# Optimization experiments

Measured on AMD Instinct MI355X. Metric: run time of the kernel, lower is better.

Reference implementation:

```python
import jax, jax.numpy as jnp
import numpy as np

B, C, D = 4, 512, 1024
N = 8           # num_experts
DFF = 4096      # GEGLU inner dim; in-projection outputs 2*DFF


def setup_inputs() -> dict:
    key = jax.random.key(0)
    ks = jax.random.split(key, 7)
    hidden_states = jax.random.normal(ks[0], (B, C, D), dtype=jnp.float32)
    # Dispatch mask: one-hot expert assignment per token (top-1 routing).
    assign = jax.random.randint(ks[1], (B, C), 0, N)
    dispatch_mask = jax.nn.one_hot(assign, N, dtype=jnp.float32)        # [B,C,N]
    # Combine mask: same sparsity pattern, scaled by a router probability.
    probs = jax.random.uniform(ks[2], (B, C, 1), dtype=jnp.float32)
    combine_mask = dispatch_mask * probs                                 # [B,C,N]
    s_in = 1.0 / np.sqrt(D)
    s_out = 1.0 / np.sqrt(DFF)
    W_in = jax.random.normal(ks[3], (N, 2 * DFF, D), dtype=jnp.float32) * s_in
    b_in = jax.random.normal(ks[4], (N, 2 * DFF), dtype=jnp.float32) * 0.01
    W_out = jax.random.normal(ks[5], (N, D, DFF), dtype=jnp.float32) * s_out
    b_out = jax.random.normal(ks[6], (N, D), dtype=jnp.float32) * 0.01
    return {"hidden_states": hidden_states, "dispatch_mask": dispatch_mask,
            "combine_mask": combine_mask, "W_in": W_in, "b_in": b_in,
            "W_out": W_out, "b_out": b_out}


def reference(hidden_states, dispatch_mask, combine_mask, W_in, b_in, W_out, b_out):
    # Dispatch: [B,C,D] x [B,C,N] -> [N,B,C,D]
    h = jnp.einsum('bcd,bcn->nbcd', hidden_states, dispatch_mask)
    # Per-expert GEGLU FFN.
    h = jnp.einsum('nbcd,nfd->nbcf', h, W_in) + b_in[:, None, None, :]   # [N,B,C,2*DFF]
    x, gate = jnp.split(h, 2, axis=-1)
    h = x * jax.nn.gelu(gate, approximate=False)                          # torch F.gelu = exact erf
    h = jnp.einsum('nbcd,nfd->nbcf', h, W_out) + b_out[:, None, None, :]  # [N,B,C,D]
    # Combine: [N,B,C,D] x [B,C,N] -> [B,C,D]
    return jnp.einsum('nbcd,bcn->bcd', h, combine_mask)
```

## Files before the change

kernel.cpp:

```cpp
#include <hip/hip_runtime.h>
#include <math.h>

#define NTOK 2048
#define DDIM 1024
#define NEXP 8
#define DFF 4096
#define TWODFF 8192

typedef __attribute__((ext_vector_type(8))) short bf16x8;
typedef __attribute__((ext_vector_type(4))) short bf16x4;
typedef __attribute__((ext_vector_type(4))) float f32x4;

__device__ __forceinline__ short f2bf(float f) {
  unsigned u = __builtin_bit_cast(unsigned, f);
  u = (u + 0x7FFFu + ((u >> 16) & 1u)) >> 16;
  return (short)u;
}

__device__ __forceinline__ unsigned pk2(float a, float b) {
  unsigned r;
  asm("v_cvt_pk_bf16_f32 %0, %1, %2" : "=v"(r) : "v"(a), "v"(b));
  return r;
}

__global__ void route_k(const float* __restrict__ disp, const float* __restrict__ comb,
                        int* __restrict__ cnt, int* __restrict__ tokl,
                        float* __restrict__ scale) {
  __shared__ int lcnt[NEXP];
  const int tid = threadIdx.x;
  if (tid < NEXP) lcnt[tid] = 0;
  __syncthreads();
  for (int i = 0; i < 8; ++i) {
    const int t = i * 256 + tid;
    const float* row = disp + (size_t)t * NEXP;
    int e = 0;
#pragma unroll
    for (int n = 1; n < NEXP; ++n) e = (row[n] > row[e]) ? n : e;
    const float p = comb[(size_t)t * NEXP + e];
    const int slot = atomicAdd(&lcnt[e], 1);
    tokl[e * NTOK + slot] = t;
    scale[t] = p;
  }
  __syncthreads();
  if (tid < NEXP) cnt[tid] = lcnt[tid];
}

__global__ __launch_bounds__(256) void gemm1_k(
    const float* __restrict__ hid, const float* __restrict__ Win,
    const float* __restrict__ bin, const int* __restrict__ cnt,
    const int* __restrict__ tokl, short* __restrict__ act) {
  const int e = blockIdx.z;
  const int Me = cnt[e];
  const int m0 = blockIdx.y * 128;
  if (m0 >= Me) return;
  const int f0 = blockIdx.x * 64;

  __shared__ short Al[2][128 * 32];
  __shared__ short Bl[2][128 * 32];
  __shared__ int tokids[128];

  const int tid = threadIdx.x;
  if (tid < 128) {
    const int r = m0 + tid;
    tokids[tid] = (r < Me) ? tokl[e * NTOK + r] : -1;
  }
  __syncthreads();

  const int r0 = tid >> 3;
  const int c0 = (tid & 7) * 4;
  const float* aP[4];
  const float* bP[4];
#pragma unroll
  for (int i = 0; i < 4; ++i) {
    const int row = i * 32 + r0;
    const int tk = tokids[row];
    aP[i] = (tk >= 0) ? (hid + (size_t)tk * DDIM + c0) : nullptr;
    const int wr = (row < 64) ? (f0 + row) : (DFF + f0 + (row - 64));
    bP[i] = Win + (size_t)e * TWODFF * DDIM + (size_t)wr * DDIM + c0;
  }

  float4 aR[4], bR[4];
  auto load_t = [&](int k0) {
#pragma unroll
    for (int i = 0; i < 4; ++i) {
      bR[i] = *(const float4*)(bP[i] + k0);
      aR[i] = aP[i] ? *(const float4*)(aP[i] + k0) : make_float4(0.f, 0.f, 0.f, 0.f);
    }
  };
  auto store_t = [&](int buf) {
#pragma unroll
    for (int i = 0; i < 4; ++i) {
      const int row = i * 32 + r0;
      const int ba = (row * 64 + (tid & 7) * 8) ^ ((row & 7) << 4);
      uint2 va, vb;
      va.x = pk2(aR[i].x, aR[i].y); va.y = pk2(aR[i].z, aR[i].w);
      vb.x = pk2(bR[i].x, bR[i].y); vb.y = pk2(bR[i].z, bR[i].w);
      *(uint2*)((char*)Al[buf] + ba) = va;
      *(uint2*)((char*)Bl[buf] + ba) = vb;
    }
  };

  const int wid = tid >> 6, lane = tid & 63;
  const int wm = (wid >> 1) * 64;
  const int wf = (wid & 1) * 32;
  const int lr = lane & 15;
  const int kbyte = (lane >> 4) * 16;

  f32x4 accx[4][2], accg[4][2];
  const f32x4 zf = {0.f, 0.f, 0.f, 0.f};
#pragma unroll
  for (int a = 0; a < 4; ++a)
#pragma unroll
    for (int b = 0; b < 2; ++b) { accx[a][b] = zf; accg[a][b] = zf; }

  load_t(0);
  store_t(0);

  for (int kt = 0; kt < 32; ++kt) {
    if (kt < 31) load_t((kt + 1) * 32);
    __syncthreads();
    const char* Ab = (const char*)Al[kt & 1];
    const char* Bb = (const char*)Bl[kt & 1];
    bf16x8 a[4], bx[2], bg[2];
#pragma unroll
    for (int fm = 0; fm < 4; ++fm) {
      const int row = wm + fm * 16 + lr;
      a[fm] = *(const bf16x8*)(Ab + ((row * 64 + kbyte) ^ ((row & 7) << 4)));
    }
#pragma unroll
    for (int ff = 0; ff < 2; ++ff) {
      const int rx = wf + ff * 16 + lr;
      bx[ff] = *(const bf16x8*)(Bb + ((rx * 64 + kbyte) ^ ((rx & 7) << 4)));
      const int rg = rx + 64;
      bg[ff] = *(const bf16x8*)(Bb + ((rg * 64 + kbyte) ^ ((rg & 7) << 4)));
    }
#pragma unroll
    for (int fm = 0; fm < 4; ++fm)
#pragma unroll
      for (int ff = 0; ff < 2; ++ff) {
        accx[fm][ff] = __builtin_amdgcn_mfma_f32_16x16x32_bf16(a[fm], bx[ff], accx[fm][ff], 0, 0, 0);
        accg[fm][ff] = __builtin_amdgcn_mfma_f32_16x16x32_bf16(a[fm], bg[ff], accg[fm][ff], 0, 0, 0);
      }
    if (kt < 31) store_t((kt + 1) & 1);
  }

  const int orb = (lane >> 4) * 4;
#pragma unroll
  for (int ff = 0; ff < 2; ++ff) {
    const int fcol = f0 + wf + ff * 16 + lr;
    const float bx_ = bin[e * TWODFF + fcol];
    const float bg_ = bin[e * TWODFF + DFF + fcol];
#pragma unroll
    for (int fm = 0; fm < 4; ++fm)
#pragma unroll
      for (int j = 0; j < 4; ++j) {
        const int row = wm + fm * 16 + orb + j;
        if (m0 + row < Me) {
          const float x = accx[fm][ff][j] + bx_;
          const float g = accg[fm][ff][j] + bg_;
          const float gl = 0.5f * g * (1.f + erff(g * 0.70710678118654752f));
          act[(size_t)tokids[row] * DFF + fcol] = f2bf(x * gl);
        }
      }
  }
}

__global__ __launch_bounds__(256) void gemm2_k(
    const short* __restrict__ act, const float* __restrict__ Wout,
    const float* __restrict__ bout, const int* __restrict__ cnt,
    const int* __restrict__ tokl, const float* __restrict__ scale,
    float* __restrict__ out) {
  const int e = blockIdx.z;
  const int Me = cnt[e];
  const int m0 = blockIdx.y * 128;
  if (m0 >= Me) return;
  const int n0 = blockIdx.x * 64;

  __shared__ short Al[2][128 * 64];
  __shared__ short Bl[2][64 * 64];
  __shared__ int tokids[128];
  __shared__ float pv[128];

  const int tid = threadIdx.x;
  if (tid < 128) {
    const int r = m0 + tid;
    const int tk = (r < Me) ? tokl[e * NTOK + r] : -1;
    tokids[tid] = tk;
    pv[tid] = (tk >= 0) ? scale[tk] : 0.f;
  }
  __syncthreads();

  const int ar0 = tid >> 3;
  const int ac0 = (tid & 7) * 8;
  const short* aP[4];
#pragma unroll
  for (int i = 0; i < 4; ++i) {
    const int row = i * 32 + ar0;
    const int tk = tokids[row];
    aP[i] = (tk >= 0) ? (act + (size_t)tk * DFF + ac0) : nullptr;
  }
  const int br0 = tid >> 4;
  const int bc0 = (tid & 15) * 4;
  const float* bP[4];
#pragma unroll
  for (int i = 0; i < 4; ++i) {
    const int row = i * 16 + br0;
    bP[i] = Wout + (size_t)e * DDIM * DFF + (size_t)(n0 + row) * DFF + bc0;
  }

  bf16x8 aR[4];
  float4 bR[4];
  auto load_t = [&](int k0) {
#pragma unroll
    for (int i = 0; i < 4; ++i) bR[i] = *(const float4*)(bP[i] + k0);
    const bf16x8 z = {0, 0, 0, 0, 0, 0, 0, 0};
#pragma unroll
    for (int i = 0; i < 4; ++i) aR[i] = aP[i] ? *(const bf16x8*)(aP[i] + k0) : z;
  };
  auto store_t = [&](int buf) {
#pragma unroll
    for (int i = 0; i < 4; ++i) {
      const int row = i * 32 + ar0;
      const int ba = (row * 128 + (tid & 7) * 16) ^ ((row & 7) << 4);
      *(bf16x8*)((char*)Al[buf] + ba) = aR[i];
    }
#pragma unroll
    for (int i = 0; i < 4; ++i) {
      const int row = i * 16 + br0;
      const int bb = (row * 128 + (tid & 15) * 8) ^ ((row & 7) << 4);
      uint2 vb;
      vb.x = pk2(bR[i].x, bR[i].y); vb.y = pk2(bR[i].z, bR[i].w);
      *(uint2*)((char*)Bl[buf] + bb) = vb;
    }
  };

  const int wid = tid >> 6, lane = tid & 63;
  const int wm = (wid >> 1) * 64;
  const int wn = (wid & 1) * 32;
  const int lr = lane & 15;
  const int lkb = (lane >> 4) * 16;

  f32x4 acc[4][2];
  const f32x4 zf = {0.f, 0.f, 0.f, 0.f};
#pragma unroll
  for (int a = 0; a < 4; ++a) { acc[a][0] = zf; acc[a][1] = zf; }

  load_t(0);
  store_t(0);

  for (int kt = 0; kt < 64; ++kt) {
    if (kt < 63) load_t((kt + 1) * 64);
    __syncthreads();
    const char* Ab = (const char*)Al[kt & 1];
    const char* Bb = (const char*)Bl[kt & 1];
#pragma unroll
    for (int ks = 0; ks < 2; ++ks) {
      bf16x8 a[4], b[2];
      const int kb = ks * 64 + lkb;
#pragma unroll
      for (int fm = 0; fm < 4; ++fm) {
        const int row = wm + fm * 16 + lr;
        a[fm] = *(const bf16x8*)(Ab + ((row * 128 + kb) ^ ((row & 7) << 4)));
      }
#pragma unroll
      for (int ff = 0; ff < 2; ++ff) {
        const int rn = wn + ff * 16 + lr;
        b[ff] = *(const bf16x8*)(Bb + ((rn * 128 + kb) ^ ((rn & 7) << 4)));
      }
#pragma unroll
      for (int fm = 0; fm < 4; ++fm)
#pragma unroll
        for (int ff = 0; ff < 2; ++ff)
          acc[fm][ff] = __builtin_amdgcn_mfma_f32_16x16x32_bf16(a[fm], b[ff], acc[fm][ff], 0, 0, 0);
    }
    if (kt < 63) store_t((kt + 1) & 1);
  }

  const int orb = (lane >> 4) * 4;
#pragma unroll
  for (int ff = 0; ff < 2; ++ff) {
    const int ncol = n0 + wn + ff * 16 + lr;
    const float bo = bout[e * DDIM + ncol];
#pragma unroll
    for (int fm = 0; fm < 4; ++fm)
#pragma unroll
      for (int j = 0; j < 4; ++j) {
        const int row = wm + fm * 16 + orb + j;
        if (m0 + row < Me)
          out[(size_t)tokids[row] * DDIM + ncol] = pv[row] * (acc[fm][ff][j] + bo);
      }
  }
}

extern "C" void kernel_launch(void* const* d_in, const int* in_sizes, int n_in,
                              void* d_out, int out_size, void* d_ws, size_t ws_size,
                              hipStream_t stream) {
  const float* hid = (const float*)d_in[0];
  const float* disp = (const float*)d_in[1];
  const float* comb = (const float*)d_in[2];
  const float* Win = (const float*)d_in[3];
  const float* bin = (const float*)d_in[4];
  const float* Wout = (const float*)d_in[5];
  const float* bout = (const float*)d_in[6];
  float* out = (float*)d_out;

  char* ws = (char*)d_ws;
  int* cnt = (int*)(ws);
  int* tokl = (int*)(ws + 256);
  float* scale = (float*)(ws + 256 + NTOK * NEXP * 4);
  short* act = (short*)(ws + (1 << 17));

  route_k<<<1, 256, 0, stream>>>(disp, comb, cnt, tokl, scale);
  gemm1_k<<<dim3(DFF / 64, 4, NEXP), 256, 0, stream>>>(hid, Win, bin, cnt, tokl, act);
  gemm2_k<<<dim3(DDIM / 64, 4, NEXP), 256, 0, stream>>>(act, Wout, bout, cnt, tokl, scale, out);
}
```

Baseline: 203.8 us.

## Enlarge expert GEMM tiles to 256 rows with 512 threads and interleave experts

Both expert GEMMs now use 512-thread blocks covering 256 token rows: 256x128 x/gate columns in the first GEMM and 256x64 in the second. The block index is remapped so consecutive blocks cycle across experts. Since roughly 256 tokens land on each expert, each weight tile is streamed by fewer row-blocks, cutting redundant fp32 weight traffic. The cost is fewer, larger blocks and higher register pressure in the first GEMM; when an expert has slightly more than 256 tokens, a second block still reads full weight tiles for few rows.

```diff
diff --git a/kernel.cpp b/kernel.cpp
--- a/kernel.cpp
+++ b/kernel.cpp
@@ -8,7 +8,6 @@
 #define TWODFF 8192
 
 typedef __attribute__((ext_vector_type(8))) short bf16x8;
-typedef __attribute__((ext_vector_type(4))) short bf16x4;
 typedef __attribute__((ext_vector_type(4))) float f32x4;
 
 __device__ __forceinline__ short f2bf(float f) {
@@ -45,22 +44,24 @@
   if (tid < NEXP) cnt[tid] = lcnt[tid];
 }
 
-__global__ __launch_bounds__(256) void gemm1_k(
+__global__ __launch_bounds__(512) void gemm1_k(
     const float* __restrict__ hid, const float* __restrict__ Win,
     const float* __restrict__ bin, const int* __restrict__ cnt,
     const int* __restrict__ tokl, short* __restrict__ act) {
-  const int e = blockIdx.z;
+  const int bid = blockIdx.x + 32 * (blockIdx.y + 2 * blockIdx.z);
+  const int e = bid & 7;
+  const int rem = bid >> 3;
+  const int f0 = (rem & 31) * 128;
+  const int m0 = (rem >> 5) * 256;
   const int Me = cnt[e];
-  const int m0 = blockIdx.y * 128;
   if (m0 >= Me) return;
-  const int f0 = blockIdx.x * 64;
-
-  __shared__ short Al[2][128 * 32];
-  __shared__ short Bl[2][128 * 32];
-  __shared__ int tokids[128];
+
+  __shared__ short Al[2][256 * 32];
+  __shared__ short Bl[2][256 * 32];
+  __shared__ int tokids[256];
 
   const int tid = threadIdx.x;
-  if (tid < 128) {
+  if (tid < 256) {
     const int r = m0 + tid;
     tokids[tid] = (r < Me) ? tokl[e * NTOK + r] : -1;
   }
@@ -72,10 +73,10 @@
   const float* bP[4];
 #pragma unroll
   for (int i = 0; i < 4; ++i) {
-    const int row = i * 32 + r0;
+    const int row = i * 64 + r0;
     const int tk = tokids[row];
     aP[i] = (tk >= 0) ? (hid + (size_t)tk * DDIM + c0) : nullptr;
-    const int wr = (row < 64) ? (f0 + row) : (DFF + f0 + (row - 64));
+    const int wr = (row < 128) ? (f0 + row) : (DFF + f0 + (row - 128));
     bP[i] = Win + (size_t)e * TWODFF * DDIM + (size_t)wr * DDIM + c0;
   }
 
@@ -90,7 +91,7 @@
   auto store_t = [&](int buf) {
 #pragma unroll
     for (int i = 0; i < 4; ++i) {
-      const int row = i * 32 + r0;
+      const int row = i * 64 + r0;
       const int ba = (row * 64 + (tid & 7) * 8) ^ ((row & 7) << 4);
       uint2 va, vb;
       va.x = pk2(aR[i].x, aR[i].y); va.y = pk2(aR[i].z, aR[i].w);
@@ -101,15 +102,15 @@
   };
 
   const int wid = tid >> 6, lane = tid & 63;
-  const int wm = (wid >> 1) * 64;
-  const int wf = (wid & 1) * 32;
+  const int mi = wid >> 2;
+  const int fi = wid & 3;
   const int lr = lane & 15;
   const int kbyte = (lane >> 4) * 16;
 
-  f32x4 accx[4][2], accg[4][2];
+  f32x4 accx[8][2], accg[8][2];
   const f32x4 zf = {0.f, 0.f, 0.f, 0.f};
 #pragma unroll
-  for (int a = 0; a < 4; ++a)
+  for (int a = 0; a < 8; ++a)
 #pragma unroll
     for (int b = 0; b < 2; ++b) { accx[a][b] = zf; accg[a][b] = zf; }
 
@@ -121,21 +122,21 @@
     __syncthreads();
     const char* Ab = (const char*)Al[kt & 1];
     const char* Bb = (const char*)Bl[kt & 1];
-    bf16x8 a[4], bx[2], bg[2];
-#pragma unroll
-    for (int fm = 0; fm < 4; ++fm) {
-      const int row = wm + fm * 16 + lr;
+    bf16x8 a[8], bx[2], bg[2];
+#pragma unroll
+    for (int fm = 0; fm < 8; ++fm) {
+      const int row = mi * 128 + fm * 16 + lr;
       a[fm] = *(const bf16x8*)(Ab + ((row * 64 + kbyte) ^ ((row & 7) << 4)));
     }
 #pragma unroll
     for (int ff = 0; ff < 2; ++ff) {
-      const int rx = wf + ff * 16 + lr;
+      const int rx = fi * 32 + ff * 16 + lr;
       bx[ff] = *(const bf16x8*)(Bb + ((rx * 64 + kbyte) ^ ((rx & 7) << 4)));
-      const int rg = rx + 64;
+      const int rg = rx + 128;
       bg[ff] = *(const bf16x8*)(Bb + ((rg * 64 + kbyte) ^ ((rg & 7) << 4)));
     }
 #pragma unroll
-    for (int fm = 0; fm < 4; ++fm)
+    for (int fm = 0; fm < 8; ++fm)
 #pragma unroll
       for (int ff = 0; ff < 2; ++ff) {
         accx[fm][ff] = __builtin_amdgcn_mfma_f32_16x16x32_bf16(a[fm], bx[ff], accx[fm][ff], 0, 0, 0);
@@ -147,14 +148,14 @@
   const int orb = (lane >> 4) * 4;
 #pragma unroll
   for (int ff = 0; ff < 2; ++ff) {
-    const int fcol = f0 + wf + ff * 16 + lr;
+    const int fcol = f0 + fi * 32 + ff * 16 + lr;
     const float bx_ = bin[e * TWODFF + fcol];
     const float bg_ = bin[e * TWODFF + DFF + fcol];
 #pragma unroll
-    for (int fm = 0; fm < 4; ++fm)
+    for (int fm = 0; fm < 8; ++fm)
 #pragma unroll
       for (int j = 0; j < 4; ++j) {
-        const int row = wm + fm * 16 + orb + j;
+        const int row = mi * 128 + fm * 16 + orb + j;
         if (m0 + row < Me) {
           const float x = accx[fm][ff][j] + bx_;
           const float g = accg[fm][ff][j] + bg_;
@@ -165,24 +166,26 @@
   }
 }
 
-__global__ __launch_bounds__(256) void gemm2_k(
+__global__ __launch_bounds__(512) void gemm2_k(
     const short* __restrict__ act, const float* __restrict__ Wout,
     const float* __restrict__ bout, const int* __restrict__ cnt,
     const int* __restrict__ tokl, const float* __restrict__ scale,
     float* __restrict__ out) {
-  const int e = blockIdx.z;
+  const int bid = blockIdx.x + 16 * (blockIdx.y + 2 * blockIdx.z);
+  const int e = bid & 7;
+  const int rem = bid >> 3;
+  const int n0 = (rem & 15) * 64;
+  const int m0 = (rem >> 4) * 256;
   const int Me = cnt[e];
-  const int m0 = blockIdx.y * 128;
   if (m0 >= Me) return;
-  const int n0 = blockIdx.x * 64;
-
-  __shared__ short Al[2][128 * 64];
+
+  __shared__ short Al[2][256 * 64];
   __shared__ short Bl[2][64 * 64];
-  __shared__ int tokids[128];
-  __shared__ float pv[128];
+  __shared__ int tokids[256];
+  __shared__ float pv[256];
 
   const int tid = threadIdx.x;
-  if (tid < 128) {
+  if (tid < 256) {
     const int r = m0 + tid;
     const int tk = (r < Me) ? tokl[e * NTOK + r] : -1;
     tokids[tid] = tk;
@@ -191,28 +194,26 @@
   __syncthreads();
 
   const int ar0 = tid >> 3;
-  const int ac0 = (tid & 7) * 8;
   const short* aP[4];
 #pragma unroll
   for (int i = 0; i < 4; ++i) {
-    const int row = i * 32 + ar0;
+    const int row = i * 64 + ar0;
     const int tk = tokids[row];
-    aP[i] = (tk >= 0) ? (act + (size_t)tk * DFF + ac0) : nullptr;
+    aP[i] = (tk >= 0) ? (act + (size_t)tk * DFF + (tid & 7) * 8) : nullptr;
   }
   const int br0 = tid >> 4;
-  const int bc0 = (tid & 15) * 4;
-  const float* bP[4];
-#pragma unroll
-  for (int i = 0; i < 4; ++i) {
-    const int row = i * 16 + br0;
-    bP[i] = Wout + (size_t)e * DDIM * DFF + (size_t)(n0 + row) * DFF + bc0;
+  const float* bP[2];
+#pragma unroll
+  for (int i = 0; i < 2; ++i) {
+    const int row = i * 32 + br0;
+    bP[i] = Wout + (size_t)e * DDIM * DFF + (size_t)(n0 + row) * DFF + (tid & 15) * 4;
   }
 
   bf16x8 aR[4];
-  float4 bR[4];
+  float4 bR[2];
   auto load_t = [&](int k0) {
 #pragma unroll
-    for (int i = 0; i < 4; ++i) bR[i] = *(const float4*)(bP[i] + k0);
+    for (int i = 0; i < 2; ++i) bR[i] = *(const float4*)(bP[i] + k0);
     const bf16x8 z = {0, 0, 0, 0, 0, 0, 0, 0};
 #pragma unroll
     for (int i = 0; i < 4; ++i) aR[i] = aP[i] ? *(const bf16x8*)(aP[i] + k0) : z;
@@ -220,13 +221,13 @@
   auto store_t = [&](int buf) {
 #pragma unroll
     for (int i = 0; i < 4; ++i) {
-      const int row = i * 32 + ar0;
+      const int row = i * 64 + ar0;
       const int ba = (row * 128 + (tid & 7) * 16) ^ ((row & 7) << 4);
       *(bf16x8*)((char*)Al[buf] + ba) = aR[i];
     }
 #pragma unroll
-    for (int i = 0; i < 4; ++i) {
-      const int row = i * 16 + br0;
+    for (int i = 0; i < 2; ++i) {
+      const int row = i * 32 + br0;
       const int bb = (row * 128 + (tid & 15) * 8) ^ ((row & 7) << 4);
       uint2 vb;
       vb.x = pk2(bR[i].x, bR[i].y); vb.y = pk2(bR[i].z, bR[i].w);
@@ -235,8 +236,8 @@
   };
 
   const int wid = tid >> 6, lane = tid & 63;
-  const int wm = (wid >> 1) * 64;
-  const int wn = (wid & 1) * 32;
+  const int mi = wid >> 1;
+  const int di = wid & 1;
   const int lr = lane & 15;
   const int lkb = (lane >> 4) * 16;
 
@@ -259,12 +260,12 @@
       const int kb = ks * 64 + lkb;
 #pragma unroll
       for (int fm = 0; fm < 4; ++fm) {
-        const int row = wm + fm * 16 + lr;
+        const int row = mi * 64 + fm * 16 + lr;
         a[fm] = *(const bf16x8*)(Ab + ((row * 128 + kb) ^ ((row & 7) << 4)));
       }
 #pragma unroll
       for (int ff = 0; ff < 2; ++ff) {
-        const int rn = wn + ff * 16 + lr;
+        const int rn = di * 32 + ff * 16 + lr;
         b[ff] = *(const bf16x8*)(Bb + ((rn * 128 + kb) ^ ((rn & 7) << 4)));
       }
 #pragma unroll
@@ -279,13 +280,13 @@
   const int orb = (lane >> 4) * 4;
 #pragma unroll
   for (int ff = 0; ff < 2; ++ff) {
-    const int ncol = n0 + wn + ff * 16 + lr;
+    const int ncol = n0 + di * 32 + ff * 16 + lr;
     const float bo = bout[e * DDIM + ncol];
 #pragma unroll
     for (int fm = 0; fm < 4; ++fm)
 #pragma unroll
       for (int j = 0; j < 4; ++j) {
-        const int row = wm + fm * 16 + orb + j;
+        const int row = mi * 64 + fm * 16 + orb + j;
         if (m0 + row < Me)
           out[(size_t)tokids[row] * DDIM + ncol] = pv[row] * (acc[fm][ff][j] + bo);
       }
@@ -311,6 +312,6 @@
   short* act = (short*)(ws + (1 << 17));
 
   route_k<<<1, 256, 0, stream>>>(disp, comb, cnt, tokl, scale);
-  gemm1_k<<<dim3(DFF / 64, 4, NEXP), 256, 0, stream>>>(hid, Win, bin, cnt, tokl, act);
-  gemm2_k<<<dim3(DDIM / 64, 4, NEXP), 256, 0, stream>>>(act, Wout, bout, cnt, tokl, scale, out);
-}
+  gemm1_k<<<dim3(32, 2, NEXP), 512, 0, stream>>>(hid, Win, bin, cnt, tokl, act);
+  gemm2_k<<<dim3(16, 2, NEXP), 512, 0, stream>>>(act, Wout, bout, cnt, tokl, scale, out);
+}
```

After: 201.9 us. Within noise of the previous version (-0.9%).

## Deepen gemm1 prefetch to triple-buffered LDS with two register stages

Applied to the files above, without the earlier changes.

The gemm1 kernel moves from double-buffered LDS with a one-tile-ahead register prefetch to three LDS buffers and two alternating register sets, so global loads are issued two k-tiles ahead. The aim is to hide more global-memory latency behind the MFMA work. It also adds a launch-bounds minimum of 3 blocks per CU, which limits registers, and it increases LDS use and register pressure, with a risk of spills. The gemm2 change is a cosmetic inlining of an offset.

```diff
diff --git a/kernel.cpp b/kernel.cpp
--- a/kernel.cpp
+++ b/kernel.cpp
@@ -8,7 +8,6 @@
 #define TWODFF 8192
 
 typedef __attribute__((ext_vector_type(8))) short bf16x8;
-typedef __attribute__((ext_vector_type(4))) short bf16x4;
 typedef __attribute__((ext_vector_type(4))) float f32x4;
 
 __device__ __forceinline__ short f2bf(float f) {
@@ -45,7 +44,25 @@
   if (tid < NEXP) cnt[tid] = lcnt[tid];
 }
 
-__global__ __launch_bounds__(256) void gemm1_k(
+#define G1_LOAD(aR, bR, k0) do {                                              \
+  _Pragma("unroll") for (int i_ = 0; i_ < 4; ++i_) {                          \
+    bR[i_] = *(const float4*)(bP[i_] + (k0));                                 \
+    aR[i_] = aP[i_] ? *(const float4*)(aP[i_] + (k0))                         \
+                    : make_float4(0.f, 0.f, 0.f, 0.f);                        \
+  } } while (0)
+
+#define G1_STORE(aR, bR, buf) do {                                            \
+  _Pragma("unroll") for (int i_ = 0; i_ < 4; ++i_) {                          \
+    const int row_ = i_ * 32 + r0;                                            \
+    const int ba_ = (row_ * 64 + (tid & 7) * 8) ^ ((row_ & 7) << 4);          \
+    uint2 va_, vb_;                                                           \
+    va_.x = pk2(aR[i_].x, aR[i_].y); va_.y = pk2(aR[i_].z, aR[i_].w);         \
+    vb_.x = pk2(bR[i_].x, bR[i_].y); vb_.y = pk2(bR[i_].z, bR[i_].w);         \
+    *(uint2*)((char*)Al[buf] + ba_) = va_;                                    \
+    *(uint2*)((char*)Bl[buf] + ba_) = vb_;                                    \
+  } } while (0)
+
+__global__ __launch_bounds__(256, 3) void gemm1_k(
     const float* __restrict__ hid, const float* __restrict__ Win,
     const float* __restrict__ bin, const int* __restrict__ cnt,
     const int* __restrict__ tokl, short* __restrict__ act) {
@@ -55,8 +72,8 @@
   if (m0 >= Me) return;
   const int f0 = blockIdx.x * 64;
 
-  __shared__ short Al[2][128 * 32];
-  __shared__ short Bl[2][128 * 32];
+  __shared__ short Al[3][128 * 32];
+  __shared__ short Bl[3][128 * 32];
   __shared__ int tokids[128];
 
   const int tid = threadIdx.x;
@@ -79,27 +96,6 @@
     bP[i] = Win + (size_t)e * TWODFF * DDIM + (size_t)wr * DDIM + c0;
   }
 
-  float4 aR[4], bR[4];
-  auto load_t = [&](int k0) {
-#pragma unroll
-    for (int i = 0; i < 4; ++i) {
-      bR[i] = *(const float4*)(bP[i] + k0);
-      aR[i] = aP[i] ? *(const float4*)(aP[i] + k0) : make_float4(0.f, 0.f, 0.f, 0.f);
-    }
-  };
-  auto store_t = [&](int buf) {
-#pragma unroll
-    for (int i = 0; i < 4; ++i) {
-      const int row = i * 32 + r0;
-      const int ba = (row * 64 + (tid & 7) * 8) ^ ((row & 7) << 4);
-      uint2 va, vb;
-      va.x = pk2(aR[i].x, aR[i].y); va.y = pk2(aR[i].z, aR[i].w);
-      vb.x = pk2(bR[i].x, bR[i].y); vb.y = pk2(bR[i].z, bR[i].w);
-      *(uint2*)((char*)Al[buf] + ba) = va;
-      *(uint2*)((char*)Bl[buf] + ba) = vb;
-    }
-  };
-
   const int wid = tid >> 6, lane = tid & 63;
   const int wm = (wid >> 1) * 64;
   const int wf = (wid & 1) * 32;
@@ -113,14 +109,16 @@
 #pragma unroll
     for (int b = 0; b < 2; ++b) { accx[a][b] = zf; accg[a][b] = zf; }
 
-  load_t(0);
-  store_t(0);
+  float4 aRa[4], bRa[4], aRb[4], bRb[4];
+  G1_LOAD(aRa, bRa, 0);
+  G1_STORE(aRa, bRa, 0);
+  G1_LOAD(aRa, bRa, 32);
+  G1_LOAD(aRb, bRb, 64);
 
   for (int kt = 0; kt < 32; ++kt) {
-    if (kt < 31) load_t((kt + 1) * 32);
     __syncthreads();
-    const char* Ab = (const char*)Al[kt & 1];
-    const char* Bb = (const char*)Bl[kt & 1];
+    const char* Ab = (const char*)Al[kt % 3];
+    const char* Bb = (const char*)Bl[kt % 3];
     bf16x8 a[4], bx[2], bg[2];
 #pragma unroll
     for (int fm = 0; fm < 4; ++fm) {
@@ -141,7 +139,16 @@
         accx[fm][ff] = __builtin_amdgcn_mfma_f32_16x16x32_bf16(a[fm], bx[ff], accx[fm][ff], 0, 0, 0);
         accg[fm][ff] = __builtin_amdgcn_mfma_f32_16x16x32_bf16(a[fm], bg[ff], accg[fm][ff], 0, 0, 0);
       }
-    if (kt < 31) store_t((kt + 1) & 1);
+    if (kt < 31) {
+      const int wb = (kt + 1) % 3;
+      if (kt & 1) {
+        G1_STORE(aRb, bRb, wb);
+        if (kt < 29) G1_LOAD(aRb, bRb, (kt + 3) * 32);
+      } else {
+        G1_STORE(aRa, bRa, wb);
+        if (kt < 29) G1_LOAD(aRa, bRa, (kt + 3) * 32);
+      }
+    }
   }
 
   const int orb = (lane >> 4) * 4;
@@ -200,12 +207,11 @@
     aP[i] = (tk >= 0) ? (act + (size_t)tk * DFF + ac0) : nullptr;
   }
   const int br0 = tid >> 4;
-  const int bc0 = (tid & 15) * 4;
   const float* bP[4];
 #pragma unroll
   for (int i = 0; i < 4; ++i) {
     const int row = i * 16 + br0;
-    bP[i] = Wout + (size_t)e * DDIM * DFF + (size_t)(n0 + row) * DFF + bc0;
+    bP[i] = Wout + (size_t)e * DDIM * DFF + (size_t)(n0 + row) * DFF + (tid & 15) * 4;
   }
 
   bf16x8 aR[4];
```

New measurement: 537.6 us. +163.8%, slower.
